# Performance work log

Hardware: AMD Instinct MI355X
Metric: run time of the kernel (lower is better)

Reference implementation:

```python
import jax, jax.numpy as jnp
import numpy as np

USER_NUM = 100000
ITEM_NUM = 50000
REC_DIM = 64
N_LAYERS = 3
N_EDGES = 2400000
N_NODES = USER_NUM + ITEM_NUM
BATCH = 4096


def setup_inputs() -> dict:
    key = jax.random.key(0)
    ks = jax.random.split(key, 7)
    user_emb = jax.random.normal(ks[0], (USER_NUM, REC_DIM), dtype=jnp.float32) * 0.1
    item_emb = jax.random.normal(ks[1], (ITEM_NUM, REC_DIM), dtype=jnp.float32) * 0.1
    edge_src = jax.random.randint(ks[2], (N_EDGES,), 0, N_NODES, dtype=jnp.int32)
    edge_dst = jax.random.randint(ks[3], (N_EDGES,), 0, N_NODES, dtype=jnp.int32)
    # symmetric-normalized adjacency values (positive)
    edge_val = jax.random.uniform(ks[4], (N_EDGES,), dtype=jnp.float32)
    users = jax.random.randint(ks[5], (BATCH,), 0, USER_NUM, dtype=jnp.int32)
    items = jax.random.randint(ks[6], (BATCH,), 0, ITEM_NUM, dtype=jnp.int32)
    return {"user_emb": user_emb, "item_emb": item_emb, "edge_src": edge_src,
            "edge_dst": edge_dst, "edge_val": edge_val, "users": users, "items": items}


def _spmm(edge_src, edge_dst, edge_val, emb):
    # out[d] = sum_{e: dst(e)=d} val(e) * emb[src(e)]   (sparse adjacency @ emb)
    msgs = edge_val[:, None] * emb[edge_src]  # [E, d]
    return jax.ops.segment_sum(msgs, edge_dst, num_segments=N_NODES)


def _propagate(user_emb, item_emb, edge_src, edge_dst, edge_val):
    e = jnp.concatenate([user_emb, item_emb], axis=0)  # [N, d]
    acc = e  # running sum instead of stack+mean
    for _ in range(N_LAYERS):
        e = _spmm(edge_src, edge_dst, edge_val, e)
        acc = acc + e
    mean = acc / float(N_LAYERS + 1)
    return mean[:USER_NUM], mean[USER_NUM:]


def reference(user_emb, item_emb, edge_src, edge_dst, edge_val, users, items):
    all_users, all_items = _propagate(user_emb, item_emb, edge_src, edge_dst, edge_val)
    users_emb = all_users[users]  # [B, d]
    items_emb = all_items[items]  # [B, d]
    gamma = jnp.sum(users_emb * items_emb, axis=1)
    return jax.nn.sigmoid(gamma)
```

## Files before the change

### kernel.cpp

```cpp
#include <hip/hip_runtime.h>
#include <hip/hip_bf16.h>
#include <hip/hip_fp16.h>

#define USER_NUM 100000
#define ITEM_NUM 50000
#define NNODES   150000
#define DIM      64
#define NEDGES   2400000
#define BATCH    4096

#define SPN      1024
#define NSUP     ((NNODES + SPN - 1) / SPN)
#define NSUPP    160
#define CHUNK    4096
#define NBLK     ((NEDGES + CHUNK - 1) / CHUNK)
#define INIT_B   ((NNODES * DIM / 4 + 255) / 256)
#define SAMP_B   ((2 * BATCH * 16 + 255) / 256)
#define SPMM_B   ((NNODES * 8 + 255) / 256)
#define MARK_B   ((2 * BATCH * 16 + 255) / 256)

__device__ inline float4 h4_to_f4(float2 raw) {
    __half2 a = ((__half2*)&raw)[0];
    __half2 b = ((__half2*)&raw)[1];
    float2 fa = __half22float2(a);
    float2 fb = __half22float2(b);
    return make_float4(fa.x, fa.y, fb.x, fb.y);
}

__device__ inline float2 f4_to_h4(float4 s) {
    __half2 a = __floats2half2_rn(s.x, s.y);
    __half2 b = __floats2half2_rn(s.z, s.w);
    float2 st;
    ((__half2*)&st)[0] = a;
    ((__half2*)&st)[1] = b;
    return st;
}

__global__ __launch_bounds__(256) void mega1_kernel(
        const int* __restrict__ edge_dst,
        int* __restrict__ bucket_cnt,
        int* __restrict__ blockhist,
        const float* __restrict__ user_emb,
        const float* __restrict__ item_emb,
        __half* __restrict__ curh,
        const int* __restrict__ users,
        const int* __restrict__ items,
        float* __restrict__ acc_s) {
    __shared__ int h[NSUP];
    int b = blockIdx.x;
    if (b < NBLK) {
        for (int t = threadIdx.x; t < NSUP; t += blockDim.x) h[t] = 0;
        __syncthreads();
        int lo = b * CHUNK;
        int hi = min(lo + CHUNK, NEDGES);
        for (int j = lo + (int)threadIdx.x; j < hi; j += blockDim.x)
            atomicAdd(&h[edge_dst[j] >> 10], 1);
        __syncthreads();
        for (int t = threadIdx.x; t < NSUP; t += blockDim.x) {
            int c = h[t];
            blockhist[b * NSUPP + t] = c;
            if (c) atomicAdd(&bucket_cnt[t], c);
        }
    } else if (b < NBLK + INIT_B) {
        const long total4 = (long)NNODES * DIM / 4;
        long i = (long)(b - NBLK) * 256 + threadIdx.x;
        if (i >= total4) return;
        const long user4 = (long)USER_NUM * DIM / 4;
        float4 v;
        if (i < user4) v = ((const float4*)user_emb)[i];
        else           v = ((const float4*)item_emb)[i - user4];
        ((float2*)curh)[i] = f4_to_h4(v);
    } else {
        int t = (b - NBLK - INIT_B) * 256 + threadIdx.x;
        int slot = t >> 4;
        if (slot >= 2 * BATCH) return;
        int k = (t & 15) * 4;
        const float* src = (slot < BATCH)
            ? &user_emb[(long)users[slot] * DIM]
            : &item_emb[(long)items[slot - BATCH] * DIM];
        *(float4*)&acc_s[(long)slot * DIM + k] = *(const float4*)&src[k];
    }
}

__global__ __launch_bounds__(1024) void partition_kernel(
        const int* __restrict__ edge_src,
        const int* __restrict__ edge_dst,
        const float* __restrict__ edge_val,
        const int* __restrict__ blockhist,
        const int* __restrict__ bucket_cnt,
        int* __restrict__ fill,
        int2* __restrict__ tmp) {
    __shared__ int cur_[NSUP];
    __shared__ int goff[NSUP];
    __shared__ long scl[256];
    __shared__ unsigned char sbkt[CHUNK];
    __shared__ int2 sout[CHUNK];
    int tid = threadIdx.x;
    int lo = blockIdx.x * CHUNK;
    int hi = min(lo + CHUNK, NEDGES);
    int n = hi - lo;

    int g = 0, c = 0;
    if (tid < NSUP) {
        g = bucket_cnt[tid];
        c = blockhist[blockIdx.x * NSUPP + tid];
    }
    if (tid < 256) scl[tid] = ((long)g << 32) | (unsigned)c;
    __syncthreads();
    for (int off = 1; off < 256; off <<= 1) {
        long t = (tid >= off && tid < 256) ? scl[tid - off] : 0;
        __syncthreads();
        if (tid < 256) scl[tid] += t;
        __syncthreads();
    }
    if (tid < NSUP) {
        long incl = scl[tid];
        int gincl = (int)(incl >> 32);
        int lincl = (int)(incl & 0xffffffffL);
        int gexcl = gincl - g;
        int lexcl = lincl - c;
        cur_[tid] = lexcl;
        goff[tid] = gexcl + (c ? atomicAdd(&fill[tid], c) : 0) - lexcl;
    }
    __syncthreads();
    for (int i = tid; i < n; i += 1024) {
        int d = edge_dst[lo + i];
        int b = d >> 10;
        int pos = atomicAdd(&cur_[b], 1);
        sout[pos] = make_int2(__float_as_int(edge_val[lo + i]),
                              edge_src[lo + i] | ((d & (SPN - 1)) << 18));
        sbkt[pos] = (unsigned char)b;
    }
    __syncthreads();
    for (int i = tid; i < n; i += 1024) {
        int b = sbkt[i];
        tmp[goff[b] + i] = sout[i];
    }
}

__global__ __launch_bounds__(1024) void local_sort_kernel(
        const int* __restrict__ bucket_cnt,
        const int2* __restrict__ tmp,
        int* __restrict__ row_ptr,
        int2* __restrict__ sedge) {
    __shared__ int gsc[256];
    __shared__ int h[SPN];
    __shared__ int sc[SPN];
    __shared__ int cur[SPN];
    __shared__ int sbase, send;
    int b = blockIdx.x;
    int tid = threadIdx.x;
    int g = (tid < NSUP) ? bucket_cnt[tid] : 0;
    if (tid < 256) gsc[tid] = g;
    __syncthreads();
    for (int off = 1; off < 256; off <<= 1) {
        int t = (tid >= off && tid < 256) ? gsc[tid - off] : 0;
        __syncthreads();
        if (tid < 256) gsc[tid] += t;
        __syncthreads();
    }
    if (tid == 0) {
        int incl = gsc[b];
        int cb = bucket_cnt[b];
        sbase = incl - cb;
        send = incl;
        if (b == 0) row_ptr[NNODES] = NEDGES;
    }
    h[tid] = 0;
    __syncthreads();
    int base = sbase, end = send;
    for (int j = base + tid; j < end; j += 1024)
        atomicAdd(&h[(tmp[j].y >> 18) & (SPN - 1)], 1);
    __syncthreads();
    int c = h[tid];
    sc[tid] = c;
    __syncthreads();
    for (int off = 1; off < SPN; off <<= 1) {
        int t = (tid >= off) ? sc[tid - off] : 0;
        __syncthreads();
        sc[tid] += t;
        __syncthreads();
    }
    int excl = sc[tid] - c;
    cur[tid] = base + excl;
    int node = b * SPN + tid;
    if (node < NNODES) row_ptr[node] = base + excl;
    __syncthreads();
    for (int j = base + tid; j < end; j += 1024) {
        int2 e = tmp[j];
        int dl = (e.y >> 18) & (SPN - 1);
        int pos = atomicAdd(&cur[dl], 1);
        sedge[pos] = make_int2(e.y & 0x3FFFF, e.x);
    }
}

__device__ inline void spmm_row(int row, int k,
                                const int* __restrict__ row_ptr,
                                const int2* __restrict__ sedge,
                                const __half* __restrict__ cur,
                                __half* __restrict__ next) {
    int start = row_ptr[row];
    int end   = row_ptr[row + 1];
    float a0[8], a1[8], a2[8], a3[8];
    #pragma unroll
    for (int q = 0; q < 8; ++q) { a0[q] = 0.f; a1[q] = 0.f; a2[q] = 0.f; a3[q] = 0.f; }
    int j = start;
    for (; j + 4 <= end; j += 4) {
        int2 e0 = sedge[j];
        int2 e1 = sedge[j + 1];
        int2 e2 = sedge[j + 2];
        int2 e3 = sedge[j + 3];
        float4 r0 = *(const float4*)&cur[(long)e0.x * DIM + k];
        float4 r1 = *(const float4*)&cur[(long)e1.x * DIM + k];
        float4 r2 = *(const float4*)&cur[(long)e2.x * DIM + k];
        float4 r3 = *(const float4*)&cur[(long)e3.x * DIM + k];
        float v0 = __int_as_float(e0.y), v1 = __int_as_float(e1.y);
        float v2 = __int_as_float(e2.y), v3 = __int_as_float(e3.y);
        const __half2* h0 = (const __half2*)&r0;
        const __half2* h1 = (const __half2*)&r1;
        const __half2* h2 = (const __half2*)&r2;
        const __half2* h3 = (const __half2*)&r3;
        #pragma unroll
        for (int q = 0; q < 4; ++q) {
            float2 f0 = __half22float2(h0[q]);
            float2 f1 = __half22float2(h1[q]);
            float2 f2 = __half22float2(h2[q]);
            float2 f3 = __half22float2(h3[q]);
            a0[2*q]   += v0 * f0.x;  a0[2*q+1] += v0 * f0.y;
            a1[2*q]   += v1 * f1.x;  a1[2*q+1] += v1 * f1.y;
            a2[2*q]   += v2 * f2.x;  a2[2*q+1] += v2 * f2.y;
            a3[2*q]   += v3 * f3.x;  a3[2*q+1] += v3 * f3.y;
        }
    }
    for (; j < end; ++j) {
        int2 e = sedge[j];
        float v = __int_as_float(e.y);
        float4 r = *(const float4*)&cur[(long)e.x * DIM + k];
        const __half2* h = (const __half2*)&r;
        #pragma unroll
        for (int q = 0; q < 4; ++q) {
            float2 f = __half22float2(h[q]);
            a0[2*q]   += v * f.x;
            a0[2*q+1] += v * f.y;
        }
    }
    float4 st;
    __half2* sh = (__half2*)&st;
    #pragma unroll
    for (int q = 0; q < 4; ++q) {
        float lo = (a0[2*q]   + a1[2*q])   + (a2[2*q]   + a3[2*q]);
        float hi = (a0[2*q+1] + a1[2*q+1]) + (a2[2*q+1] + a3[2*q+1]);
        sh[q] = __floats2half2_rn(lo, hi);
    }
    *(float4*)&next[(long)row * DIM + k] = st;
}

__global__ void spmm_mark_kernel(const int* __restrict__ row_ptr,
                                 const int2* __restrict__ sedge,
                                 const __half* __restrict__ cur,
                                 __half* __restrict__ next,
                                 const int* __restrict__ users,
                                 const int* __restrict__ items,
                                 int* __restrict__ flags) {
    if (blockIdx.x < SPMM_B) {
        long t = (long)blockIdx.x * 256 + threadIdx.x;
        int row = (int)(t >> 3);
        if (row >= NNODES) return;
        spmm_row(row, ((int)t & 7) * 8, row_ptr, sedge, cur, next);
    } else {
        int t = (blockIdx.x - SPMM_B) * 256 + threadIdx.x;
        int slot = t >> 4;
        if (slot >= 2 * BATCH) return;
        int lane16 = t & 15;
        int node = (slot < BATCH) ? users[slot] : USER_NUM + items[slot - BATCH];
        if (lane16 == 0) flags[node] = 1;
        int start = row_ptr[node];
        int end   = row_ptr[node + 1];
        for (int j = start + lane16; j < end; j += 16)
            flags[sedge[j].x] = 1;
    }
}

__global__ void spmm_flag_sa_kernel(const int* __restrict__ row_ptr,
                                    const int2* __restrict__ sedge,
                                    const __half* __restrict__ cur,
                                    __half* __restrict__ next,
                                    const int* __restrict__ users,
                                    const int* __restrict__ items,
                                    float* __restrict__ acc_s,
                                    const int* __restrict__ flags) {
    if (blockIdx.x < SPMM_B) {
        long t = (long)blockIdx.x * 256 + threadIdx.x;
        int row = (int)(t >> 3);
        if (row >= NNODES) return;
        if (!flags[row]) return;
        spmm_row(row, ((int)t & 7) * 8, row_ptr, sedge, cur, next);
    } else {
        int t = (blockIdx.x - SPMM_B) * 256 + threadIdx.x;
        int slot = t >> 4;
        if (slot >= 2 * BATCH) return;
        int k = (t & 15) * 4;
        int node = (slot < BATCH) ? users[slot] : USER_NUM + items[slot - BATCH];
        float4 x = h4_to_f4(*(const float2*)&cur[(long)node * DIM + k]);
        long o = (long)slot * DIM + k;
        float4 a = *(float4*)&acc_s[o];
        a.x += x.x; a.y += x.y; a.z += x.z; a.w += x.w;
        *(float4*)&acc_s[o] = a;
    }
}

__global__ __launch_bounds__(256) void pair_kernel(
        const int* __restrict__ row_ptr,
        const int2* __restrict__ sedge,
        const __half* __restrict__ tab,
        const int* __restrict__ users,
        const int* __restrict__ items,
        const float* __restrict__ acc_s,
        float* __restrict__ out) {
    int t = blockIdx.x * 256 + threadIdx.x;
    int p = t >> 5;
    if (p >= BATCH) return;
    int sub = t & 31;
    int lane = threadIdx.x & 63;
    bool isU = (sub < 16);
    int k = (sub & 15) * 4;
    int node = isU ? users[p] : USER_NUM + items[p];
    int slot = isU ? p : BATCH + p;

    int start = row_ptr[node];
    int end   = row_ptr[node + 1];
    float4 s0 = make_float4(0.f, 0.f, 0.f, 0.f);
    float4 s1 = s0;
    int j = start;
    for (; j + 2 <= end; j += 2) {
        int2 e0 = sedge[j];
        int2 e1 = sedge[j + 1];
        float4 x0 = h4_to_f4(*(const float2*)&tab[(long)e0.x * DIM + k]);
        float4 x1 = h4_to_f4(*(const float2*)&tab[(long)e1.x * DIM + k]);
        float v0 = __int_as_float(e0.y), v1 = __int_as_float(e1.y);
        s0.x += v0 * x0.x; s0.y += v0 * x0.y; s0.z += v0 * x0.z; s0.w += v0 * x0.w;
        s1.x += v1 * x1.x; s1.y += v1 * x1.y; s1.z += v1 * x1.z; s1.w += v1 * x1.w;
    }
    for (; j < end; ++j) {
        int2 e = sedge[j];
        float v = __int_as_float(e.y);
        float4 x = h4_to_f4(*(const float2*)&tab[(long)e.x * DIM + k]);
        s0.x += v * x.x; s0.y += v * x.y; s0.z += v * x.z; s0.w += v * x.w;
    }
    float4 a = *(const float4*)&acc_s[(long)slot * DIM + k];
    float4 e2v = h4_to_f4(*(const float2*)&tab[(long)node * DIM + k]);
    a.x += e2v.x + s0.x + s1.x;
    a.y += e2v.y + s0.y + s1.y;
    a.z += e2v.z + s0.z + s1.z;
    a.w += e2v.w + s0.w + s1.w;

    int partner = (lane + 16) & 63;
    float bx = __shfl(a.x, partner);
    float by = __shfl(a.y, partner);
    float bz = __shfl(a.z, partner);
    float bw = __shfl(a.w, partner);
    float pd = a.x * bx + a.y * by + a.z * bz + a.w * bw;
    #pragma unroll
    for (int off = 1; off < 16; off <<= 1) pd += __shfl_xor(pd, off);
    if (sub == 0) {
        float gamma = pd * (1.0f / 16.0f);
        out[p] = 1.0f / (1.0f + __expf(-gamma));
    }
}

extern "C" void kernel_launch(void* const* d_in, const int* in_sizes, int n_in,
                              void* d_out, int out_size, void* d_ws, size_t ws_size,
                              hipStream_t stream) {
    const float* user_emb = (const float*)d_in[0];
    const float* item_emb = (const float*)d_in[1];
    const int*   edge_src = (const int*)d_in[2];
    const int*   edge_dst = (const int*)d_in[3];
    const float* edge_val = (const float*)d_in[4];
    const int*   users    = (const int*)d_in[5];
    const int*   items    = (const int*)d_in[6];
    float* out = (float*)d_out;

    const size_t tbl  = (size_t)NNODES * DIM * sizeof(float);
    const size_t htbl = (size_t)NNODES * DIM * sizeof(__half);
    char* w = (char*)d_ws;
    float*  acc_s       = (float*)w;   w += tbl;
    char*   bufA        = w;           w += tbl;
    char*   bufB        = w;           w += tbl;
    int2*   sedge       = (int2*)w;    w += (size_t)NEDGES * 8;
    int*    row_ptr     = (int*)w;     w += ((size_t)NNODES + 16) * 4;
    int*    bucket_cnt  = (int*)w;     w += ((size_t)NSUP + 8) * 4;
    int*    fill        = (int*)w;     w += ((size_t)NSUP + 8) * 4;
    int*    flags       = (int*)w;     w += (size_t)NNODES * 4;
    const size_t zero_bytes = (size_t)((char*)w - (char*)bucket_cnt);
    int*    blockhist   = (int*)w;     w += (size_t)NBLK * NSUPP * 4;

    int2*   tmp   = (int2*)bufA;
    __half* tabA  = (__half*)bufB;
    __half* tabB  = (__half*)(bufB + htbl);

    hipMemsetAsync(bucket_cnt, 0, zero_bytes, stream);
    mega1_kernel<<<NBLK + INIT_B + SAMP_B, 256, 0, stream>>>(
        edge_dst, bucket_cnt, blockhist,
        user_emb, item_emb, tabA, users, items, acc_s);
    partition_kernel<<<NBLK, 1024, 0, stream>>>(edge_src, edge_dst, edge_val,
                                                blockhist, bucket_cnt, fill, tmp);
    local_sort_kernel<<<NSUP, 1024, 0, stream>>>(bucket_cnt, tmp, row_ptr, sedge);
    spmm_mark_kernel<<<SPMM_B + MARK_B, 256, 0, stream>>>(
        row_ptr, sedge, tabA, tabB, users, items, flags);
    spmm_flag_sa_kernel<<<SPMM_B + SAMP_B, 256, 0, stream>>>(
        row_ptr, sedge, tabB, tabA, users, items, acc_s, flags);
    pair_kernel<<<(BATCH * 32 + 255) / 256, 256, 0, stream>>>(
        row_ptr, sedge, tabA, users, items, acc_s, out);
}
```

Before: 191.2 us.

## Fuse CSR build stages into one cooperative kernel with grid syncs

Merges the histogram/init, partition, and local-sort kernels into a single cooperative launch of 256 blocks of 1024 threads. Grid-wide syncs separate the phases, and each block now handles a larger edge chunk of about 9375 edges. This removes two kernel launch boundaries and their tail effects. The cost is fewer, bigger blocks with more shared memory (the sout array grows to about 75KB), which may limit occupancy, plus grid-sync overhead and the requirement that all blocks are co-resident.

Measured after the change: 262.7 us. 37.4% more time.

```diff
diff --git a/kernel.cpp b/kernel.cpp
--- a/kernel.cpp
+++ b/kernel.cpp
@@ -1,6 +1,9 @@
 #include <hip/hip_runtime.h>
 #include <hip/hip_bf16.h>
 #include <hip/hip_fp16.h>
+#include <hip/hip_cooperative_groups.h>
+
+namespace cg = cooperative_groups;
 
 #define USER_NUM 100000
 #define ITEM_NUM 50000
@@ -12,11 +15,10 @@
 #define SPN      1024
 #define NSUP     ((NNODES + SPN - 1) / SPN)
 #define NSUPP    160
-#define CHUNK    4096
-#define NBLK     ((NEDGES + CHUNK - 1) / CHUNK)
-#define INIT_B   ((NNODES * DIM / 4 + 255) / 256)
+#define NBLK_C   256
+#define CHUNK_C  (NEDGES / NBLK_C)
+#define SPMM_B   ((NNODES * 8 + 255) / 256)
 #define SAMP_B   ((2 * BATCH * 16 + 255) / 256)
-#define SPMM_B   ((NNODES * 8 + 255) / 256)
 #define MARK_B   ((2 * BATCH * 16 + 255) / 256)
 
 __device__ inline float4 h4_to_f4(float2 raw) {
@@ -36,161 +38,149 @@
     return st;
 }
 
-__global__ __launch_bounds__(256) void mega1_kernel(
+__global__ __launch_bounds__(1024) void csr_coop_kernel(
+        const int* __restrict__ edge_src,
         const int* __restrict__ edge_dst,
+        const float* __restrict__ edge_val,
+        const float* __restrict__ user_emb,
+        const float* __restrict__ item_emb,
+        const int* __restrict__ users,
+        const int* __restrict__ items,
         int* __restrict__ bucket_cnt,
         int* __restrict__ blockhist,
-        const float* __restrict__ user_emb,
-        const float* __restrict__ item_emb,
-        __half* __restrict__ curh,
-        const int* __restrict__ users,
-        const int* __restrict__ items,
+        int* __restrict__ fill,
+        int2* __restrict__ tmp,
+        int* __restrict__ row_ptr,
+        int2* __restrict__ sedge,
+        __half* __restrict__ tabA,
         float* __restrict__ acc_s) {
-    __shared__ int h[NSUP];
+    __shared__ int2 sout[CHUNK_C];
+    __shared__ unsigned char sbkt[CHUNK_C];
+    __shared__ int cur_[NSUP];
+    __shared__ int goff[NSUP];
+    __shared__ long scl[256];
+    __shared__ int h2[SPN];
+    __shared__ int sc2[SPN];
+    __shared__ int cur2[SPN];
+    __shared__ int gsc[256];
+    __shared__ int sbase, send;
+
+    cg::grid_group grid = cg::this_grid();
     int b = blockIdx.x;
-    if (b < NBLK) {
-        for (int t = threadIdx.x; t < NSUP; t += blockDim.x) h[t] = 0;
-        __syncthreads();
-        int lo = b * CHUNK;
-        int hi = min(lo + CHUNK, NEDGES);
-        for (int j = lo + (int)threadIdx.x; j < hi; j += blockDim.x)
-            atomicAdd(&h[edge_dst[j] >> 10], 1);
-        __syncthreads();
-        for (int t = threadIdx.x; t < NSUP; t += blockDim.x) {
-            int c = h[t];
-            blockhist[b * NSUPP + t] = c;
-            if (c) atomicAdd(&bucket_cnt[t], c);
-        }
-    } else if (b < NBLK + INIT_B) {
-        const long total4 = (long)NNODES * DIM / 4;
-        long i = (long)(b - NBLK) * 256 + threadIdx.x;
-        if (i >= total4) return;
-        const long user4 = (long)USER_NUM * DIM / 4;
+    int tid = threadIdx.x;
+    int lo = b * CHUNK_C;
+
+    for (int t = tid; t < NSUP; t += 1024) cur_[t] = 0;
+    __syncthreads();
+    for (int j = lo + tid; j < lo + CHUNK_C; j += 1024)
+        atomicAdd(&cur_[edge_dst[j] >> 10], 1);
+    __syncthreads();
+    for (int t = tid; t < NSUP; t += 1024) {
+        int c = cur_[t];
+        blockhist[b * NSUPP + t] = c;
+        if (c) atomicAdd(&bucket_cnt[t], c);
+    }
+    const long total4 = (long)NNODES * DIM / 4;
+    const long user4  = (long)USER_NUM * DIM / 4;
+    for (long i = (long)b * 1024 + tid; i < total4; i += (long)NBLK_C * 1024) {
         float4 v;
         if (i < user4) v = ((const float4*)user_emb)[i];
         else           v = ((const float4*)item_emb)[i - user4];
-        ((float2*)curh)[i] = f4_to_h4(v);
-    } else {
-        int t = (b - NBLK - INIT_B) * 256 + threadIdx.x;
+        ((float2*)tabA)[i] = f4_to_h4(v);
+    }
+    for (int t = b * 1024 + tid; t < 2 * BATCH * 16; t += NBLK_C * 1024) {
         int slot = t >> 4;
-        if (slot >= 2 * BATCH) return;
         int k = (t & 15) * 4;
         const float* src = (slot < BATCH)
             ? &user_emb[(long)users[slot] * DIM]
             : &item_emb[(long)items[slot - BATCH] * DIM];
         *(float4*)&acc_s[(long)slot * DIM + k] = *(const float4*)&src[k];
     }
-}
-
-__global__ __launch_bounds__(1024) void partition_kernel(
-        const int* __restrict__ edge_src,
-        const int* __restrict__ edge_dst,
-        const float* __restrict__ edge_val,
-        const int* __restrict__ blockhist,
-        const int* __restrict__ bucket_cnt,
-        int* __restrict__ fill,
-        int2* __restrict__ tmp) {
-    __shared__ int cur_[NSUP];
-    __shared__ int goff[NSUP];
-    __shared__ long scl[256];
-    __shared__ unsigned char sbkt[CHUNK];
-    __shared__ int2 sout[CHUNK];
-    int tid = threadIdx.x;
-    int lo = blockIdx.x * CHUNK;
-    int hi = min(lo + CHUNK, NEDGES);
-    int n = hi - lo;
-
-    int g = 0, c = 0;
-    if (tid < NSUP) {
-        g = bucket_cnt[tid];
-        c = blockhist[blockIdx.x * NSUPP + tid];
-    }
-    if (tid < 256) scl[tid] = ((long)g << 32) | (unsigned)c;
-    __syncthreads();
-    for (int off = 1; off < 256; off <<= 1) {
-        long t = (tid >= off && tid < 256) ? scl[tid - off] : 0;
-        __syncthreads();
-        if (tid < 256) scl[tid] += t;
-        __syncthreads();
-    }
-    if (tid < NSUP) {
-        long incl = scl[tid];
-        int gincl = (int)(incl >> 32);
-        int lincl = (int)(incl & 0xffffffffL);
-        int gexcl = gincl - g;
-        int lexcl = lincl - c;
-        cur_[tid] = lexcl;
-        goff[tid] = gexcl + (c ? atomicAdd(&fill[tid], c) : 0) - lexcl;
-    }
-    __syncthreads();
-    for (int i = tid; i < n; i += 1024) {
-        int d = edge_dst[lo + i];
-        int b = d >> 10;
-        int pos = atomicAdd(&cur_[b], 1);
-        sout[pos] = make_int2(__float_as_int(edge_val[lo + i]),
-                              edge_src[lo + i] | ((d & (SPN - 1)) << 18));
-        sbkt[pos] = (unsigned char)b;
-    }
-    __syncthreads();
-    for (int i = tid; i < n; i += 1024) {
-        int b = sbkt[i];
-        tmp[goff[b] + i] = sout[i];
-    }
-}
-
-__global__ __launch_bounds__(1024) void local_sort_kernel(
-        const int* __restrict__ bucket_cnt,
-        const int2* __restrict__ tmp,
-        int* __restrict__ row_ptr,
-        int2* __restrict__ sedge) {
-    __shared__ int gsc[256];
-    __shared__ int h[SPN];
-    __shared__ int sc[SPN];
-    __shared__ int cur[SPN];
-    __shared__ int sbase, send;
-    int b = blockIdx.x;
-    int tid = threadIdx.x;
-    int g = (tid < NSUP) ? bucket_cnt[tid] : 0;
-    if (tid < 256) gsc[tid] = g;
-    __syncthreads();
-    for (int off = 1; off < 256; off <<= 1) {
-        int t = (tid >= off && tid < 256) ? gsc[tid - off] : 0;
-        __syncthreads();
-        if (tid < 256) gsc[tid] += t;
-        __syncthreads();
-    }
-    if (tid == 0) {
-        int incl = gsc[b];
-        int cb = bucket_cnt[b];
-        sbase = incl - cb;
-        send = incl;
-        if (b == 0) row_ptr[NNODES] = NEDGES;
-    }
-    h[tid] = 0;
-    __syncthreads();
-    int base = sbase, end = send;
-    for (int j = base + tid; j < end; j += 1024)
-        atomicAdd(&h[(tmp[j].y >> 18) & (SPN - 1)], 1);
-    __syncthreads();
-    int c = h[tid];
-    sc[tid] = c;
-    __syncthreads();
-    for (int off = 1; off < SPN; off <<= 1) {
-        int t = (tid >= off) ? sc[tid - off] : 0;
-        __syncthreads();
-        sc[tid] += t;
-        __syncthreads();
-    }
-    int excl = sc[tid] - c;
-    cur[tid] = base + excl;
-    int node = b * SPN + tid;
-    if (node < NNODES) row_ptr[node] = base + excl;
-    __syncthreads();
-    for (int j = base + tid; j < end; j += 1024) {
-        int2 e = tmp[j];
-        int dl = (e.y >> 18) & (SPN - 1);
-        int pos = atomicAdd(&cur[dl], 1);
-        sedge[pos] = make_int2(e.y & 0x3FFFF, e.x);
+    grid.sync();
+
+    {
+        int g = 0, c = 0;
+        if (tid < NSUP) {
+            g = bucket_cnt[tid];
+            c = blockhist[b * NSUPP + tid];
+        }
+        if (tid < 256) scl[tid] = ((long)g << 32) | (unsigned)c;
+        __syncthreads();
+        for (int off = 1; off < 256; off <<= 1) {
+            long t = (tid >= off && tid < 256) ? scl[tid - off] : 0;
+            __syncthreads();
+            if (tid < 256) scl[tid] += t;
+            __syncthreads();
+        }
+        if (tid < NSUP) {
+            long incl = scl[tid];
+            int gincl = (int)(incl >> 32);
+            int lincl = (int)(incl & 0xffffffffL);
+            int gexcl = gincl - g;
+            int lexcl = lincl - c;
+            cur_[tid] = lexcl;
+            goff[tid] = gexcl + (c ? atomicAdd(&fill[tid], c) : 0) - lexcl;
+        }
+        __syncthreads();
+        for (int i = tid; i < CHUNK_C; i += 1024) {
+            int d = edge_dst[lo + i];
+            int bb = d >> 10;
+            int pos = atomicAdd(&cur_[bb], 1);
+            sout[pos] = make_int2(__float_as_int(edge_val[lo + i]),
+                                  edge_src[lo + i] | ((d & (SPN - 1)) << 18));
+            sbkt[pos] = (unsigned char)bb;
+        }
+        __syncthreads();
+        for (int i = tid; i < CHUNK_C; i += 1024) {
+            int bb = sbkt[i];
+            tmp[goff[bb] + i] = sout[i];
+        }
+    }
+    grid.sync();
+
+    if (b < NSUP) {
+        int g = (tid < NSUP) ? bucket_cnt[tid] : 0;
+        if (tid < 256) gsc[tid] = g;
+        __syncthreads();
+        for (int off = 1; off < 256; off <<= 1) {
+            int t = (tid >= off && tid < 256) ? gsc[tid - off] : 0;
+            __syncthreads();
+            if (tid < 256) gsc[tid] += t;
+            __syncthreads();
+        }
+        if (tid == 0) {
+            int incl = gsc[b];
+            int cb = bucket_cnt[b];
+            sbase = incl - cb;
+            send = incl;
+            if (b == 0) row_ptr[NNODES] = NEDGES;
+        }
+        h2[tid] = 0;
+        __syncthreads();
+        int base = sbase, end = send;
+        for (int j = base + tid; j < end; j += 1024)
+            atomicAdd(&h2[(tmp[j].y >> 18) & (SPN - 1)], 1);
+        __syncthreads();
+        int c = h2[tid];
+        sc2[tid] = c;
+        __syncthreads();
+        for (int off = 1; off < SPN; off <<= 1) {
+            int t = (tid >= off) ? sc2[tid - off] : 0;
+            __syncthreads();
+            sc2[tid] += t;
+            __syncthreads();
+        }
+        int excl = sc2[tid] - c;
+        cur2[tid] = base + excl;
+        int node = b * SPN + tid;
+        if (node < NNODES) row_ptr[node] = base + excl;
+        __syncthreads();
+        for (int j = base + tid; j < end; j += 1024) {
+            int2 e = tmp[j];
+            int dl = (e.y >> 18) & (SPN - 1);
+            int pos = atomicAdd(&cur2[dl], 1);
+            sedge[pos] = make_int2(e.y & 0x3FFFF, e.x);
+        }
     }
 }
 
@@ -371,11 +361,11 @@
 extern "C" void kernel_launch(void* const* d_in, const int* in_sizes, int n_in,
                               void* d_out, int out_size, void* d_ws, size_t ws_size,
                               hipStream_t stream) {
-    const float* user_emb = (const float*)d_in[0];
-    const float* item_emb = (const float*)d_in[1];
     const int*   edge_src = (const int*)d_in[2];
     const int*   edge_dst = (const int*)d_in[3];
     const float* edge_val = (const float*)d_in[4];
+    const float* user_emb = (const float*)d_in[0];
+    const float* item_emb = (const float*)d_in[1];
     const int*   users    = (const int*)d_in[5];
     const int*   items    = (const int*)d_in[6];
     float* out = (float*)d_out;
@@ -392,19 +382,24 @@
     int*    fill        = (int*)w;     w += ((size_t)NSUP + 8) * 4;
     int*    flags       = (int*)w;     w += (size_t)NNODES * 4;
     const size_t zero_bytes = (size_t)((char*)w - (char*)bucket_cnt);
-    int*    blockhist   = (int*)w;     w += (size_t)NBLK * NSUPP * 4;
+    int*    blockhist   = (int*)w;     w += (size_t)NBLK_C * NSUPP * 4;
 
     int2*   tmp   = (int2*)bufA;
     __half* tabA  = (__half*)bufB;
     __half* tabB  = (__half*)(bufB + htbl);
 
     hipMemsetAsync(bucket_cnt, 0, zero_bytes, stream);
-    mega1_kernel<<<NBLK + INIT_B + SAMP_B, 256, 0, stream>>>(
-        edge_dst, bucket_cnt, blockhist,
-        user_emb, item_emb, tabA, users, items, acc_s);
-    partition_kernel<<<NBLK, 1024, 0, stream>>>(edge_src, edge_dst, edge_val,
-                                                blockhist, bucket_cnt, fill, tmp);
-    local_sort_kernel<<<NSUP, 1024, 0, stream>>>(bucket_cnt, tmp, row_ptr, sedge);
+
+    void* args[] = {
+        (void*)&edge_src, (void*)&edge_dst, (void*)&edge_val,
+        (void*)&user_emb, (void*)&item_emb, (void*)&users, (void*)&items,
+        (void*)&bucket_cnt, (void*)&blockhist, (void*)&fill,
+        (void*)&tmp, (void*)&row_ptr, (void*)&sedge,
+        (void*)&tabA, (void*)&acc_s
+    };
+    hipLaunchCooperativeKernel((void*)csr_coop_kernel, dim3(NBLK_C), dim3(1024),
+                               args, 0, stream);
+
     spmm_mark_kernel<<<SPMM_B + MARK_B, 256, 0, stream>>>(
         row_ptr, sedge, tabA, tabB, users, items, flags);
     spmm_flag_sa_kernel<<<SPMM_B + SAMP_B, 256, 0, stream>>>(
```
